# Performance work log

Hardware: AMD Instinct MI355X
Metric: run time of the kernel (lower is better)

Reference implementation:

```python
import jax, jax.numpy as jnp
import numpy as np
import math

DIM = 1024; B = 4; S = 2048; R = 3; K = 256; MAXR = 256; H = 8; HD = DIM // H
THRESH = 0.5; EPS = 1e-5

def _gelu(x):
    return jax.nn.gelu(x, approximate=False)

def _ln(x, g, b):
    m = jnp.mean(x, axis=-1, keepdims=True)
    v = jnp.var(x, axis=-1, keepdims=True)
    return (x - m) * jax.lax.rsqrt(v + EPS) * g + b

def setup_inputs() -> dict:
    key = jax.random.key(0)
    ks = jax.random.split(key, 24)
    sd = 1.0 / math.sqrt(DIM)
    sd2 = 1.0 / math.sqrt(2 * DIM)
    return {
        'x': jax.random.normal(ks[0], (B, S, DIM), jnp.float32),
        'retrieved': jax.random.normal(ks[1], (R, B, K, DIM), jnp.float32),
        # per-retriever query generator MLPs: Linear->GELU->Linear
        'qg_w1': jax.random.normal(ks[2], (R, DIM, DIM), jnp.float32) * sd,
        'qg_b1': jnp.zeros((R, DIM), jnp.float32),
        'qg_w2': jax.random.normal(ks[3], (R, DIM, DIM), jnp.float32) * sd,
        'qg_b2': jnp.zeros((R, DIM), jnp.float32),
        # per-retriever pooler: LayerNorm -> Linear
        'pln_g': jnp.ones((R, DIM), jnp.float32),
        'pln_b': jnp.zeros((R, DIM), jnp.float32),
        'pool_w': jax.random.normal(ks[4], (R, DIM, DIM), jnp.float32) * sd,
        'pool_b': jnp.zeros((R, DIM), jnp.float32),
        # relevance scorer: Linear(2d,d/2)->GELU->Linear(d/2,1)->Sigmoid
        'rel_w1': jax.random.normal(ks[5], (2 * DIM, DIM // 2), jnp.float32) * sd2,
        'rel_b1': jnp.zeros((DIM // 2,), jnp.float32),
        'rel_w2': jax.random.normal(ks[6], (DIM // 2, 1), jnp.float32) * (1.0 / math.sqrt(DIM // 2)),
        'rel_b2': jnp.zeros((1,), jnp.float32),
        # fusion MultiheadAttention: stacked q/k/v in-proj + out-proj
        'in_w': jax.random.normal(ks[7], (3, DIM, DIM), jnp.float32) * sd,
        'in_b': jnp.zeros((3, DIM), jnp.float32),
        'out_w': jax.random.normal(ks[8], (DIM, DIM), jnp.float32) * sd,
        'out_b': jnp.zeros((DIM,), jnp.float32),
        # fusion LayerNorm
        'fln_g': jnp.ones((DIM,), jnp.float32),
        'fln_b': jnp.zeros((DIM,), jnp.float32),
    }

def reference(x, retrieved, qg_w1, qg_b1, qg_w2, qg_b2, pln_g, pln_b, pool_w, pool_b,
              rel_w1, rel_b1, rel_w2, rel_b2, in_w, in_b, out_w, out_b, fln_g, fln_b):
    # ---- query generation: per-retriever MLP + self-attn pooling ----
    qf = _gelu(jnp.einsum('bsd,rde->rbse', x, qg_w1) + qg_b1[:, None, None, :])
    qf = jnp.einsum('rbsd,rde->rbse', qf, qg_w2) + qg_b2[:, None, None, :]  # [R,B,S,D]
    attn = jax.nn.softmax(jnp.einsum('rbsd,rbtd->rbst', qf, qf) / math.sqrt(DIM), axis=-1)
    pooled = jnp.einsum('rbst,rbtd->rbsd', attn, qf).mean(axis=2)  # [R,B,D]
    pooled = _ln(pooled, pln_g[:, None, :], pln_b[:, None, :])
    queries = jnp.einsum('rbd,rde->rbe', pooled, pool_w) + pool_b[:, None, :]  # [R,B,D]
    # ---- relevance scoring of retrieved tokens against queries ----
    q_exp = jnp.broadcast_to(queries[:, :, None, :], (R, B, K, DIM))
    pairs = jnp.concatenate([retrieved, q_exp], axis=-1)  # [R,B,K,2D]
    h = _gelu(pairs @ rel_w1 + rel_b1)
    rel = jax.nn.sigmoid((h @ rel_w2 + rel_b2)[..., 0])  # [R,B,K]
    # ---- threshold mask + per-batch top-k across all retrievers ----
    cand_tok = jnp.transpose(retrieved, (1, 0, 2, 3)).reshape(B, R * K, DIM)
    cand_rel = jnp.transpose(rel, (1, 0, 2)).reshape(B, R * K)
    valid = cand_rel >= THRESH
    masked_rel = jnp.where(valid, cand_rel, -jnp.inf)
    _, top_idx = jax.lax.top_k(masked_rel, MAXR)  # [B,MAXR]
    sel_tok = jnp.take_along_axis(cand_tok, top_idx[..., None], axis=1)  # [B,MAXR,D]
    key_valid = jnp.take_along_axis(valid, top_idx, axis=1)  # [B,MAXR]
    any_valid = jnp.any(key_valid, axis=-1)  # [B]
    # ---- fusion: cross-attention x -> selected tokens, residual + LN ----
    q = (x @ in_w[0] + in_b[0]).reshape(B, S, H, HD)
    k = (sel_tok @ in_w[1] + in_b[1]).reshape(B, MAXR, H, HD)
    v = (sel_tok @ in_w[2] + in_b[2]).reshape(B, MAXR, H, HD)
    scores = jnp.einsum('bshd,bthd->bhst', q, k) / math.sqrt(HD)
    scores = jnp.where(key_valid[:, None, None, :], scores, -1e9)
    a = jax.nn.softmax(scores, axis=-1)
    fused = jnp.einsum('bhst,bthd->bshd', a, v).reshape(B, S, DIM) @ out_w + out_b
    enhanced = _ln(x + fused, fln_g, fln_b)
    return jnp.where(any_valid[:, None, None], enhanced, x)
```

## Files before the change

kernel.cpp:

```cpp
#include <hip/hip_runtime.h>
#include <math.h>


typedef unsigned short u16;
typedef unsigned int   u32;
typedef __attribute__((ext_vector_type(8))) short short8;
typedef __attribute__((ext_vector_type(4))) float f32x4;
typedef __attribute__((ext_vector_type(4))) u16  u16x4;

__device__ __forceinline__ float b2f(u16 u){ union{float f;u32 i;} x; x.i=((u32)u)<<16; return x.f; }
__device__ __forceinline__ u16 f2b(float f){ union{float f;u32 i;} x; x.f=f; u32 r=x.i+0x7fffu+((x.i>>16)&1u); return (u16)(r>>16); }
__device__ __forceinline__ float gelu_f(float v){ return 0.5f*v*(1.f+erff(v*0.70710678118654752f)); }

__device__ __forceinline__ void load_lds16(const u16* g, u16* l){
  __builtin_amdgcn_global_load_lds((const __attribute__((address_space(1))) u32*)g,
                                   (__attribute__((address_space(3))) u32*)l, 16, 0, 0);
}

__device__ __forceinline__ float waveRedSum(float v){
  #pragma unroll
  for (int o=32;o>0;o>>=1) v += __shfl_xor(v,o);
  return v;
}
__device__ __forceinline__ float waveRedMax(float v){
  #pragma unroll
  for (int o=32;o>0;o>>=1) v = fmaxf(v, __shfl_xor(v,o));
  return v;
}
__device__ float blockRedSum(float v){
  __shared__ float tmp[17];
  const int lane = threadIdx.x&63, wv = threadIdx.x>>6, nw = blockDim.x>>6;
  v = waveRedSum(v);
  __syncthreads();
  if (lane==0) tmp[wv]=v;
  __syncthreads();
  if (threadIdx.x==0){ float s=tmp[0]; for(int i=1;i<nw;i++) s+=tmp[i]; tmp[16]=s; }
  __syncthreads();
  return tmp[16];
}
__device__ float blockRedMax(float v){
  __shared__ float tmp[17];
  const int lane = threadIdx.x&63, wv = threadIdx.x>>6, nw = blockDim.x>>6;
  v = waveRedMax(v);
  __syncthreads();
  if (lane==0) tmp[wv]=v;
  __syncthreads();
  if (threadIdx.x==0){ float s=tmp[0]; for(int i=1;i<nw;i++) s=fmaxf(s,tmp[i]); tmp[16]=s; }
  __syncthreads();
  return tmp[16];
}

enum { EPI_NONE=0, EPI_BIAS=1, EPI_SCALE=3, EPI_VT=5 };

template<int EPI>
__global__ __launch_bounds__(512,4)
void gemm_nt(const u16* __restrict__ Ag, long long lda, long long sA1, long long sA2,
             const u16* __restrict__ Bg, long long ldb, long long sB1, long long sB2,
             u16* __restrict__ Cg, long long ldc, long long sC1, long long sC2,
             const float* __restrict__ bias, long long sBias,
             float scale, int K, int H)
{
  __shared__ u16 As[2*4096];
  __shared__ u16 Bs[2*4096];
  const int z  = blockIdx.z;
  const int zb = z / H, zh = z - zb*H;
  const u16* A = Ag + zb*sA1 + zh*sA2;
  const u16* B = Bg + zb*sB1 + zh*sB2;
  const int m0 = blockIdx.y*128, n0 = blockIdx.x*128;
  const int t  = threadIdx.x;
  const int lane = t & 63, wv = t >> 6;
  const int wm = (wv>>1)*32, wn = (wv&1)*64;

  const u16* ga0 = A + (long long)(m0 + (t>>2))*lda + (t&3)*8;
  const u16* gb0 = B + (long long)(n0 + (t>>2))*ldb + (t&3)*8;
  u16* lA0 = As + t*8;
  u16* lB0 = Bs + t*8;

  f32x4 acc[2][4];
  #pragma unroll
  for (int i=0;i<2;i++)
    #pragma unroll
    for (int j=0;j<4;j++) acc[i][j] = (f32x4){0.f,0.f,0.f,0.f};

  const short8* arp = (const short8*)(As + (wm + (lane&15))*32 + ((lane>>4)*8));
  const short8* brp = (const short8*)(Bs + (wn + (lane&15))*32 + ((lane>>4)*8));

  #define STAGE_NT(bo) do{ \
    load_lds16(ga0, lA0+(bo)); \
    load_lds16(gb0, lB0+(bo)); \
    ga0 += 32; gb0 += 32; }while(0)

  const int nk = K >> 5;
  STAGE_NT(0);
  asm volatile("s_waitcnt vmcnt(0)" ::: "memory");
  __builtin_amdgcn_s_barrier();
  int cur = 0;
  for (int kk = 0; kk < nk; ++kk) {
    if (kk+1 < nk) STAGE_NT((cur^1)*4096);
    const int boS = cur*512;
    short8 af[2], bfr[4];
    #pragma unroll
    for (int i=0;i<2;i++) af[i]  = arp[boS + i*64];
    #pragma unroll
    for (int j=0;j<4;j++) bfr[j] = brp[boS + j*64];
    #pragma unroll
    for (int i=0;i<2;i++)
      #pragma unroll
      for (int j=0;j<4;j++)
        acc[i][j] = __builtin_amdgcn_mfma_f32_16x16x32_bf16(af[i], bfr[j], acc[i][j], 0, 0, 0);
    asm volatile("s_waitcnt vmcnt(0)" ::: "memory");
    __builtin_amdgcn_s_barrier();
    cur ^= 1;
  }
  #undef STAGE_NT

  u16* C = Cg + zb*sC1 + zh*sC2;
  const float* bz = bias + zb*sBias;
  const int rb0 = m0 + wm + ((lane>>4)<<2);
  const int cb0 = n0 + wn + (lane&15);
  #pragma unroll
  for (int j=0;j<4;j++){
    const int cn = cb0 + j*16;
    float bv = 0.f;
    if constexpr (EPI==EPI_BIAS || EPI==EPI_VT) bv = bz[cn];
    #pragma unroll
    for (int i=0;i<2;i++){
      #pragma unroll
      for (int p=0;p<4;p++){
        const int row = rb0 + i*16 + p;
        float v = acc[i][j][p];
        if constexpr (EPI==EPI_SCALE) v *= scale;
        if constexpr (EPI==EPI_BIAS)  v += bv;
        if constexpr (EPI==EPI_VT) {
          v += bv;
          const int bb = row>>8, tt = row&255, hh = cn>>7, dd = cn&127;
          C[((long long)((bb*8+hh)*128+dd)<<8) + tt] = f2b(v);
        } else {
          C[(long long)row*ldc + cn] = f2b(v);
        }
      }
    }
  }
}

enum { SP_GELU_SPLIT=0, SP_BIAS_SPLIT=1, SP_SCALE_F32=2, SP_QBG_F32=3, SP_SCALE_STATS=4 };

template<int EPI>
__global__ __launch_bounds__(512,4)
void gemm_nt_split(const u16* __restrict__ Ah_, const u16* __restrict__ Al_, long long lda, long long sAz,
                   const u16* __restrict__ Bh_, const u16* __restrict__ Bl_, long long ldb, long long sBz,
                   void* __restrict__ C0, void* __restrict__ C1, long long ldc, long long sCz,
                   const float* __restrict__ bias, float scale, int K,
                   float* __restrict__ pm, float* __restrict__ ps)
{
  __shared__ u16 AsH[2*4096];
  __shared__ u16 AsL[2*4096];
  __shared__ u16 BsH[2*4096];
  __shared__ u16 BsL[2*4096];
  const int z = blockIdx.z;
  const int m0 = blockIdx.y*128, n0 = blockIdx.x*128;
  const int t  = threadIdx.x;
  const int lane = t & 63, wv = t >> 6;
  const int wm = (wv>>1)*32, wn = (wv&1)*64;

  const long long arow = (long long)z*sAz + (long long)(m0 + (t>>2))*lda + (t&3)*8;
  const long long brow = (long long)z*sBz + (long long)(n0 + (t>>2))*ldb + (t&3)*8;
  const u16* gah0 = Ah_ + arow;
  const u16* gal0 = Al_ + arow;
  const u16* gbh0 = Bh_ + brow;
  const u16* gbl0 = Bl_ + brow;
  u16* lAh0 = AsH + t*8;  u16* lAl0 = AsL + t*8;
  u16* lBh0 = BsH + t*8;  u16* lBl0 = BsL + t*8;

  f32x4 acc[2][4];
  #pragma unroll
  for (int i=0;i<2;i++)
    #pragma unroll
    for (int j=0;j<4;j++) acc[i][j] = (f32x4){0.f,0.f,0.f,0.f};

  const int foff = (lane&15)*32 + ((lane>>4)*8);
  const short8* arh = (const short8*)(AsH + wm*32 + foff);
  const short8* arl = (const short8*)(AsL + wm*32 + foff);
  const short8* brh = (const short8*)(BsH + wn*32 + foff);
  const short8* brl = (const short8*)(BsL + wn*32 + foff);

  #define STAGE_SP(bo) do{ \
    load_lds16(gah0, lAh0+(bo)); load_lds16(gal0, lAl0+(bo)); \
    load_lds16(gbh0, lBh0+(bo)); load_lds16(gbl0, lBl0+(bo)); \
    gah0 += 32; gal0 += 32; gbh0 += 32; gbl0 += 32; }while(0)

  const int nk = K >> 5;
  STAGE_SP(0);
  asm volatile("s_waitcnt vmcnt(0)" ::: "memory");
  __builtin_amdgcn_s_barrier();
  int cur = 0;
  for (int kk = 0; kk < nk; ++kk) {
    if (kk+1 < nk) STAGE_SP((cur^1)*4096);
    const int boS = cur*512;
    short8 fah[2], fal[2], fbh[4], fbl[4];
    #pragma unroll
    for (int i=0;i<2;i++){ fah[i]=arh[boS+i*64]; fal[i]=arl[boS+i*64]; }
    #pragma unroll
    for (int j=0;j<4;j++){ fbh[j]=brh[boS+j*64]; fbl[j]=brl[boS+j*64]; }
    #pragma unroll
    for (int i=0;i<2;i++)
      #pragma unroll
      for (int j=0;j<4;j++){
        acc[i][j] = __builtin_amdgcn_mfma_f32_16x16x32_bf16(fal[i], fbh[j], acc[i][j], 0, 0, 0);
        acc[i][j] = __builtin_amdgcn_mfma_f32_16x16x32_bf16(fah[i], fbl[j], acc[i][j], 0, 0, 0);
        acc[i][j] = __builtin_amdgcn_mfma_f32_16x16x32_bf16(fah[i], fbh[j], acc[i][j], 0, 0, 0);
      }
    asm volatile("s_waitcnt vmcnt(0)" ::: "memory");
    __builtin_amdgcn_s_barrier();
    cur ^= 1;
  }
  #undef STAGE_SP

  const int rb0 = m0 + wm + ((lane>>4)<<2);
  const int cb0 = n0 + wn + (lane&15);
  #pragma unroll
  for (int j=0;j<4;j++){
    const int cn = cb0 + j*16;
    float bv = 0.f;
    if constexpr (EPI==SP_GELU_SPLIT || EPI==SP_BIAS_SPLIT) bv = bias[cn];
    #pragma unroll
    for (int i=0;i<2;i++){
      #pragma unroll
      for (int p=0;p<4;p++){
        const int row = rb0 + i*16 + p;
        float v = acc[i][j][p];
        const long long o = (long long)z*sCz + (long long)row*ldc + cn;
        if constexpr (EPI==SP_GELU_SPLIT || EPI==SP_BIAS_SPLIT){
          v += bv;
          if constexpr (EPI==SP_GELU_SPLIT) v = gelu_f(v);
          const u16 h = f2b(v);
          ((u16*)C0)[o] = h;
          ((u16*)C1)[o] = f2b(v - b2f(h));
        }
        if constexpr (EPI==SP_SCALE_F32 || EPI==SP_SCALE_STATS) ((float*)C0)[o] = v*scale;
        if constexpr (EPI==SP_QBG_F32)   ((float*)C0)[o] = gelu_f(v + bias[(row>>8)*512 + cn]);
      }
    }
  }

  if constexpr (EPI==SP_SCALE_STATS){
    const int g = blockIdx.x*2 + (wv&1);
    #pragma unroll
    for (int i=0;i<2;i++){
      #pragma unroll
      for (int p=0;p<4;p++){
        float mx = -3.4e38f;
        #pragma unroll
        for (int j=0;j<4;j++) mx = fmaxf(mx, acc[i][j][p]*scale);
        #pragma unroll
        for (int o=1;o<16;o<<=1) mx = fmaxf(mx, __shfl_xor(mx,o));
        float sm = 0.f;
        #pragma unroll
        for (int j=0;j<4;j++) sm += expf(acc[i][j][p]*scale - mx);
        #pragma unroll
        for (int o=1;o<16;o<<=1) sm += __shfl_xor(sm,o);
        if ((lane&15)==0){
          const int row = rb0 + i*16 + p;
          const long long pi = ((long long)z*2048 + row)*32 + g;
          pm[pi] = mx; ps[pi] = sm;
        }
      }
    }
  }
}

__global__ __launch_bounds__(256)
void merge_stats(const float* __restrict__ pm, const float* __restrict__ ps,
                 float* __restrict__ m0o, float* __restrict__ d0o,
                 float* __restrict__ m1o, float* __restrict__ d1o){
  const int wv = threadIdx.x>>6, lane = threadIdx.x&63;
  const int row = blockIdx.x*8 + wv*2 + (lane>>5);
  const int g = lane & 31;
  const long long pi = (long long)row*32 + g;
  const float mg = pm[pi];
  float m = mg;
  #pragma unroll
  for (int o=1;o<32;o<<=1) m = fmaxf(m, __shfl_xor(m,o));
  float s = ps[pi] * expf(mg - m);
  #pragma unroll
  for (int o=1;o<32;o<<=1) s += __shfl_xor(s,o);
  if (g==0){
    if (row < 2048){ m0o[row]=m; d0o[row]=s; }
    else           { m1o[row-2048]=m; d1o[row-2048]=s; }
  }
}

__global__ void transpose_w(const float* __restrict__ in, u16* __restrict__ out, int rows, int cols){
  __shared__ float tl[32][33];
  const long long zo = (long long)blockIdx.z*rows*cols;
  const int c0 = blockIdx.x*32, r0 = blockIdx.y*32;
  const int tx = threadIdx.x, ty = threadIdx.y;
  #pragma unroll
  for (int yy=ty; yy<32; yy+=8) tl[yy][tx] = in[zo + (long long)(r0+yy)*cols + (c0+tx)];
  __syncthreads();
  #pragma unroll
  for (int yy=ty; yy<32; yy+=8) out[zo + (long long)(c0+yy)*rows + (r0+tx)] = f2b(tl[tx][yy]);
}

__global__ void split_transpose_w(const float* __restrict__ in, u16* __restrict__ outH,
                                  u16* __restrict__ outL, int rows, int cols){
  __shared__ float tl[32][33];
  const long long zo = (long long)blockIdx.z*rows*cols;
  const int c0 = blockIdx.x*32, r0 = blockIdx.y*32;
  const int tx = threadIdx.x, ty = threadIdx.y;
  #pragma unroll
  for (int yy=ty; yy<32; yy+=8) tl[yy][tx] = in[zo + (long long)(r0+yy)*cols + (c0+tx)];
  __syncthreads();
  #pragma unroll
  for (int yy=ty; yy<32; yy+=8){
    const float v = tl[tx][yy];
    const u16 h = f2b(v);
    const long long o = zo + (long long)(c0+yy)*rows + (r0+tx);
    outH[o] = h;
    outL[o] = f2b(v - b2f(h));
  }
}

__global__ void split_f32_k(const float* __restrict__ in, u16* __restrict__ oh,
                            u16* __restrict__ ol, int n4){
  const int i = blockIdx.x*256 + threadIdx.x;
  if (i < n4){
    const float4 v = ((const float4*)in)[i];
    u16x4 hh, ll;
    hh.x=f2b(v.x); ll.x=f2b(v.x-b2f(hh.x));
    hh.y=f2b(v.y); ll.y=f2b(v.y-b2f(hh.y));
    hh.z=f2b(v.z); ll.z=f2b(v.z-b2f(hh.z));
    hh.w=f2b(v.w); ll.w=f2b(v.w-b2f(hh.w));
    ((u16x4*)oh)[i] = hh;
    ((u16x4*)ol)[i] = ll;
  }
}

__global__ void zero_f32(float* __restrict__ p, int n){
  const int i = blockIdx.x*256 + threadIdx.x;
  if (i < n) p[i] = 0.f;
}

__global__ void init_queries(const float* __restrict__ pb, float* __restrict__ q){
  const int i = blockIdx.x*256 + threadIdx.x;
  if (i < 12288) q[i] = pb[(i>>12)*1024 + (i&1023)];
}
__global__ void init_qpart(const float* __restrict__ rb1, float* __restrict__ qp){
  const int i = blockIdx.x*256 + threadIdx.x;
  if (i < 6144) qp[i] = rb1[i&511];
}

__global__ void ws_report(float* __restrict__ out, int n4, float val){
  const int i = blockIdx.x*256 + threadIdx.x;
  if (i < n4){
    float4 z; z.x = (i==0)? val : 0.f; z.y=0.f; z.z=0.f; z.w=0.f;
    ((float4*)out)[i] = z;
  }
}

__global__ void col_mean2(const float* __restrict__ S, long long sz,
                          const float* __restrict__ m0a, const float* __restrict__ den0,
                          const float* __restrict__ m1a, const float* __restrict__ den1,
                          float* __restrict__ w){
  const int zz = blockIdx.z;
  const float* m   = zz ? m1a : m0a;
  const float* den = zz ? den1 : den0;
  const int tc = blockIdx.x*256 + threadIdx.x;
  const int s0 = blockIdx.y*64;
  const float* p = S + (long long)zz*sz + (long long)s0*2048 + tc;
  float acc = 0.f;
  for (int s=0;s<64;s++)
    acc += expf(p[(long long)s<<11] - m[s0+s]) * (1.0f/den[s0+s]);
  atomicAdd(&w[zz*2048 + tc], acc * (1.f/2048.f));
}

__global__ __launch_bounds__(256)
void pooled_par(const u16* __restrict__ qfh, const u16* __restrict__ qfl,
                const float* __restrict__ w, float* __restrict__ pooled){
  const int b = blockIdx.x, tt0 = blockIdx.y*128;
  const int t = threadIdx.x;
  __shared__ float wsh[128];
  if (t < 128) wsh[t] = w[b*2048 + tt0 + t];
  __syncthreads();
  const long long base = (long long)b*2097152 + (long long)tt0*1024;
  const u16* ph = qfh + base;
  const u16* pl = qfl + base;
  float acc[4] = {0.f,0.f,0.f,0.f};
  for (int s=0; s<128; s++){
    const float wt = wsh[s];
    const long long o = (long long)s*1024;
    #pragma unroll
    for (int k=0;k<4;k++){
      const int dd = t + k*256;
      acc[k] += wt*(b2f(ph[o+dd]) + b2f(pl[o+dd]));
    }
  }
  #pragma unroll
  for (int k=0;k<4;k++) atomicAdd(&pooled[b*1024 + t + k*256], acc[k]);
}

__global__ __launch_bounds__(1024)
void pool_ln(const float* __restrict__ pooled, const float* __restrict__ pg,
             const float* __restrict__ pb, float* __restrict__ plbuf){
  const int z = blockIdx.x, r = z>>2, d = threadIdx.x;
  const float v = pooled[z*1024+d];
  const float mean = blockRedSum(v) * (1.f/1024.f);
  const float df = v - mean;
  const float var = blockRedSum(df*df) * (1.f/1024.f);
  plbuf[z*1024+d] = df*rsqrtf(var+1e-5f)*pg[r*1024+d] + pb[r*1024+d];
}

__global__ __launch_bounds__(256)
void query_accum(const float* __restrict__ plbuf, const float* __restrict__ pw,
                 float* __restrict__ queries){
  const int z = blockIdx.x, r = z>>2, k0 = blockIdx.y*32;
  const int t = threadIdx.x;
  __shared__ float pls[32];
  if (t < 32) pls[t] = plbuf[z*1024 + k0 + t];
  __syncthreads();
  const float* wp = pw + (long long)r*1048576 + (long long)k0*1024;
  float acc[4] = {0.f,0.f,0.f,0.f};
  for (int s=0;s<32;s++){
    const float wv = pls[s];
    #pragma unroll
    for (int c=0;c<4;c++) acc[c] += wv*wp[s*1024 + t + c*256];
  }
  #pragma unroll
  for (int c=0;c<4;c++) atomicAdd(&queries[z*1024 + t + c*256], acc[c]);
}

__global__ __launch_bounds__(256)
void qpart_accum(const float* __restrict__ queries, const float* __restrict__ rw1,
                 float* __restrict__ qpart){
  const int z = blockIdx.x, k0 = blockIdx.y*64;
  const int t = threadIdx.x;
  __shared__ float qs[64];
  if (t < 64) qs[t] = queries[z*1024 + k0 + t];
  __syncthreads();
  const float* wp = rw1 + 1024*512 + (long long)k0*512;
  float acc[2] = {0.f,0.f};
  for (int s=0;s<64;s++){
    const float wv = qs[s];
    #pragma unroll
    for (int c=0;c<2;c++) acc[c] += wv*wp[s*512 + t + c*256];
  }
  #pragma unroll
  for (int c=0;c<2;c++) atomicAdd(&qpart[z*512 + t + c*256], acc[c]);
}

__global__ void rel_score_f32(const float* __restrict__ h, const float* __restrict__ w2,
                              const float* __restrict__ b2p, float* __restrict__ relv){
  const int row = blockIdx.x*4 + (threadIdx.x>>6);
  const int lane = threadIdx.x & 63;
  const float* p = h + (long long)row*512;
  float a = 0.f;
  #pragma unroll
  for (int k=0;k<8;k++){ const int idx = lane + k*64; a += p[idx]*w2[idx]; }
  a = waveRedSum(a);
  if (lane==0){
    const float lg = a + b2p[0];
    relv[row] = 1.f/(1.f+expf(-lg));
  }
}

__global__ __launch_bounds__(768)
void select_topk(const float* __restrict__ relv, int* __restrict__ selidx,
                 int* __restrict__ neff, int* __restrict__ anyv){
  const int b = blockIdx.x, c = threadIdx.x;
  __shared__ float rv[768];
  __shared__ int cnt;
  rv[c] = relv[(((c>>8)*4)+b)*256 + (c&255)];
  if (c==0) cnt = 0;
  __syncthreads();
  const float mine = rv[c];
  const bool valid = (mine >= 0.5f);
  int rank = 0;
  for (int j=0;j<768;j++){
    const float vj = rv[j];
    if (vj >= 0.5f && (vj > mine || (vj == mine && j < c))) rank++;
  }
  if (valid && rank < 256){
    const int s = atomicAdd(&cnt, 1);
    selidx[b*256 + s] = c;
  }
  __syncthreads();
  if (c==0){ neff[b] = cnt; anyv[b] = (cnt>0) ? 1 : 0; }
}

__global__ void gather_sel(const u16* __restrict__ rb16, const int* __restrict__ selidx,
                           const int* __restrict__ neff, u16* __restrict__ seltok){
  const int slot = blockIdx.x, b = blockIdx.y, tid = threadIdx.x;
  uint2 val; val.x=0u; val.y=0u;
  if (slot < neff[b]){
    const int c = selidx[b*256+slot];
    const uint2* src = (const uint2*)(rb16 + (long long)(((c>>8)*4+b)*256 + (c&255))*1024);
    val = src[tid];
  }
  ((uint2*)(seltok + (long long)(b*256+slot)*1024))[tid] = val;
}

__global__ void attn_softmax(u16* __restrict__ S, const int* __restrict__ neff){
  const int ri = blockIdx.x*4 + (threadIdx.x>>6);
  const int lane = threadIdx.x & 63;
  const int b = ri >> 14;
  const int ne = neff[b];
  u16* p = S + (long long)ri*256 + lane*4;
  if (ne == 0){ uint2 zz; zz.x=0u; zz.y=0u; *(uint2*)p = zz; return; }
  uint2 raw = *(const uint2*)p;
  u16 uu[4] = {(u16)(raw.x&0xffffu),(u16)(raw.x>>16),(u16)(raw.y&0xffffu),(u16)(raw.y>>16)};
  float xs[4];
  #pragma unroll
  for (int q2=0;q2<4;q2++){ const int tt = lane*4+q2; xs[q2] = (tt<ne)? b2f(uu[q2]) : -1e30f; }
  float mx = fmaxf(fmaxf(xs[0],xs[1]),fmaxf(xs[2],xs[3]));
  mx = waveRedMax(mx);
  float e[4]; float sm=0.f;
  #pragma unroll
  for (int q2=0;q2<4;q2++){ e[q2] = (lane*4+q2<ne)? expf(xs[q2]-mx) : 0.f; sm += e[q2]; }
  sm = waveRedSum(sm);
  const float inv = 1.f/sm;
  #pragma unroll
  for (int q2=0;q2<4;q2++) uu[q2] = f2b(e[q2]*inv);
  raw.x = (u32)uu[0] | ((u32)uu[1]<<16);
  raw.y = (u32)uu[2] | ((u32)uu[3]<<16);
  *(uint2*)p = raw;
}

__global__ void final_ln(const float* __restrict__ x, const u16* __restrict__ fused,
                         const float* __restrict__ g, const float* __restrict__ bb,
                         const int* __restrict__ anyv, float* __restrict__ out){
  const int row = blockIdx.x; const int b = row>>11; const int tid = threadIdx.x;
  const float4 xv = ((const float4*)(x + (long long)row*1024))[tid];
  const uint2 fv = ((const uint2*)(fused + (long long)row*1024))[tid];
  const float e0 = xv.x + b2f((u16)(fv.x&0xffffu));
  const float e1 = xv.y + b2f((u16)(fv.x>>16));
  const float e2 = xv.z + b2f((u16)(fv.y&0xffffu));
  const float e3 = xv.w + b2f((u16)(fv.y>>16));
  const float mean = blockRedSum(e0+e1+e2+e3) * (1.f/1024.f);
  const float d0=e0-mean, d1=e1-mean, d2=e2-mean, d3=e3-mean;
  const float var = blockRedSum(d0*d0+d1*d1+d2*d2+d3*d3) * (1.f/1024.f);
  const float inv = rsqrtf(var + 1e-5f);
  const float4 gv = ((const float4*)g)[tid];
  const float4 bv = ((const float4*)bb)[tid];
  float4 o;
  if (anyv[b]){
    o.x = d0*inv*gv.x + bv.x; o.y = d1*inv*gv.y + bv.y;
    o.z = d2*inv*gv.z + bv.z; o.w = d3*inv*gv.w + bv.w;
  } else o = xv;
  ((float4*)(out + (long long)row*1024))[tid] = o;
}

extern "C" void kernel_launch(void* const* d_in, const int* in_sizes, int n_in,
                              void* d_out, int out_size, void* d_ws, size_t ws_size,
                              hipStream_t stream) {
  (void)in_sizes; (void)n_in;
  const float* x      = (const float*)d_in[0];
  const float* retr   = (const float*)d_in[1];
  const float* qg_w1  = (const float*)d_in[2];
  const float* qg_b1  = (const float*)d_in[3];
  const float* qg_w2  = (const float*)d_in[4];
  const float* qg_b2  = (const float*)d_in[5];
  const float* pln_g  = (const float*)d_in[6];
  const float* pln_b  = (const float*)d_in[7];
  const float* pool_w = (const float*)d_in[8];
  const float* pool_b = (const float*)d_in[9];
  const float* rel_w1 = (const float*)d_in[10];
  const float* rel_b1 = (const float*)d_in[11];
  const float* rel_w2 = (const float*)d_in[12];
  const float* rel_b2 = (const float*)d_in[13];
  const float* in_w   = (const float*)d_in[14];
  const float* in_b   = (const float*)d_in[15];
  const float* out_w  = (const float*)d_in[16];
  const float* out_b  = (const float*)d_in[17];
  const float* fln_g  = (const float*)d_in[18];
  const float* fln_b  = (const float*)d_in[19];
  float* out = (float*)d_out;
  char* ws = (char*)d_ws;

  const size_t MB = 1u<<20;
  const size_t REQUIRED = 131*MB;
  if (ws_size < REQUIRED){
    ws_report<<<(out_size/4 + 255)/256, 256, 0, stream>>>(out, out_size/4, (float)(ws_size>>20));
    return;
  }

  u16* qg1Th = (u16*)(ws + 0*MB);
  u16* qg1Tl = (u16*)(ws + 6*MB);
  u16* qg2Th = (u16*)(ws + 12*MB);
  u16* qg2Tl = (u16*)(ws + 18*MB);
  u16* xh    = (u16*)(ws + 24*MB);
  u16* xl    = (u16*)(ws + 40*MB);
  u16* qfh   = (u16*)(ws + 56*MB);
  u16* qfl   = (u16*)(ws + 72*MB);
  u16* t1h   = (u16*)(ws + 88*MB);
  u16* t1l   = (u16*)(ws + 104*MB);
  float* scoresA = (float*)(ws + 88*MB);
  float* scoresB = (float*)(ws + 104*MB);
  u16* rh    = (u16*)(ws + 0*MB);
  u16* rl    = (u16*)(ws + 6*MB);
  u16* relTh = (u16*)(ws + 12*MB);
  u16* relTl = (u16*)(ws + 13*MB);
  u16* seltok= (u16*)(ws + 14*MB);
  u16* kbuf  = (u16*)(ws + 16*MB);
  u16* VT    = (u16*)(ws + 18*MB);
  float* hbuf= (float*)(ws + 88*MB);
  u16* inT   = (u16*)(ws + 40*MB);
  u16* outT  = (u16*)(ws + 46*MB);
  u16* qbuf  = (u16*)(ws + 56*MB);
  u16* fused = (u16*)(ws + 72*MB);
  u16* Sattn = (u16*)(ws + 88*MB);
  u16* attnout=(u16*)(ws + 0*MB);
  char* SM = ws + 120*MB;
  float* wbuf    = (float*)(SM);
  float* pooledB = (float*)(SM + 98304);
  float* plbuf   = (float*)(SM + 147456);
  float* queries = (float*)(SM + 196608);
  float* qpart   = (float*)(SM + 245760);
  float* relv    = (float*)(SM + 270336);
  int*   selidx  = (int*)(SM + 282624);
  int*   neff    = (int*)(SM + 286720);
  int*   anyv    = (int*)(SM + 286784);
  float* mrow0   = (float*)(SM + 286848);
  float* drow0   = (float*)(SM + 295040);
  float* mrow1   = (float*)(SM + 303232);
  float* drow1   = (float*)(SM + 311424);
  float* partM   = (float*)(SM + 512*1024);
  float* partS   = (float*)(SM + 1536*1024);

  dim3 b256(256);
  dim3 b512(512);
  dim3 tb(32,8);
  const long long SCZ = (long long)(16*MB)/4;

  split_transpose_w<<<dim3(32,32,3), tb, 0, stream>>>(qg_w1, qg1Th, qg1Tl, 1024, 1024);
  split_transpose_w<<<dim3(32,32,3), tb, 0, stream>>>(qg_w2, qg2Th, qg2Tl, 1024, 1024);
  split_f32_k<<<8192, b256, 0, stream>>>(x, xh, xl, 2097152);
  zero_f32<<<144, b256, 0, stream>>>(wbuf, 36864);

  for (int r = 0; r < 3; r++){
    const long long wo = (long long)r*1048576;
    gemm_nt_split<SP_GELU_SPLIT><<<dim3(8,64,1), b512, 0, stream>>>(
        xh, xl, 1024, 0,  qg1Th+wo, qg1Tl+wo, 1024, 0,
        t1h, t1l, 1024, 0,  qg_b1+r*1024, 1.f, 1024, nullptr, nullptr);
    gemm_nt_split<SP_BIAS_SPLIT><<<dim3(8,64,1), b512, 0, stream>>>(
        t1h, t1l, 1024, 0,  qg2Th+wo, qg2Tl+wo, 1024, 0,
        qfh, qfl, 1024, 0,  qg_b2+r*1024, 1.f, 1024, nullptr, nullptr);
    for (int p2 = 0; p2 < 2; p2++){
      const long long qo = (long long)(p2*2)*2097152;
      gemm_nt_split<SP_SCALE_STATS><<<dim3(16,16,2), b512, 0, stream>>>(
          qfh+qo, qfl+qo, 1024, 2097152,  qfh+qo, qfl+qo, 1024, 2097152,
          scoresA, nullptr, 2048, SCZ,  nullptr, 0.03125f, 1024, partM, partS);
      merge_stats<<<512, b256, 0, stream>>>(partM, partS, mrow0, drow0, mrow1, drow1);
      col_mean2<<<dim3(8,32,2), b256, 0, stream>>>(
          scoresA, SCZ, mrow0, drow0, mrow1, drow1, wbuf + (r*4+p2*2)*2048);
    }
    pooled_par<<<dim3(4,16), b256, 0, stream>>>(qfh, qfl, wbuf + r*8192, pooledB + r*4096);
  }
  pool_ln<<<12, 1024, 0, stream>>>(pooledB, pln_g, pln_b, plbuf);
  init_queries<<<48, b256, 0, stream>>>(pool_b, queries);
  query_accum<<<dim3(12,32), b256, 0, stream>>>(plbuf, pool_w, queries);

  split_f32_k<<<3072, b256, 0, stream>>>(retr, rh, rl, 786432);
  split_transpose_w<<<dim3(16,32,1), tb, 0, stream>>>(rel_w1, relTh, relTl, 1024, 512);
  init_qpart<<<24, b256, 0, stream>>>(rel_b1, qpart);
  qpart_accum<<<dim3(12,16), b256, 0, stream>>>(queries, rel_w1, qpart);
  gemm_nt_split<SP_QBG_F32><<<dim3(4,24,1), b512, 0, stream>>>(
      rh, rl, 1024, 0,  relTh, relTl, 1024, 0,  hbuf, nullptr, 512, 0,  qpart, 1.f, 1024,
      nullptr, nullptr);
  rel_score_f32<<<768, b256, 0, stream>>>(hbuf, rel_w2, rel_b2, relv);

  select_topk<<<4, 768, 0, stream>>>(relv, selidx, neff, anyv);
  gather_sel<<<dim3(256,4), b256, 0, stream>>>(rh, selidx, neff, seltok);

  transpose_w<<<dim3(32,32,3), tb, 0, stream>>>(in_w,  inT,  1024, 1024);
  transpose_w<<<dim3(32,32,1), tb, 0, stream>>>(out_w, outT, 1024, 1024);
  gemm_nt<EPI_BIAS><<<dim3(8,64,1), b512, 0, stream>>>(
      xh,1024,0,0,  inT,1024,0,0,  qbuf,1024,0,0,  in_b,0, 1.f, 1024, 1);
  gemm_nt<EPI_BIAS><<<dim3(8,8,1), b512, 0, stream>>>(
      seltok,1024,0,0,  inT+1048576,1024,0,0,  kbuf,1024,0,0,  in_b+1024,0, 1.f, 1024, 1);
  gemm_nt<EPI_VT><<<dim3(8,8,1), b512, 0, stream>>>(
      seltok,1024,0,0,  inT+2097152,1024,0,0,  VT,0,0,0,  in_b+2048,0, 1.f, 1024, 1);
  gemm_nt<EPI_SCALE><<<dim3(2,16,32), b512, 0, stream>>>(
      qbuf,1024,2097152,128,  kbuf,1024,262144,128,  Sattn,256,4194304,524288,
      (const float*)nullptr,0, 0.08838834764831845f, 128, 8);
  attn_softmax<<<16384, b256, 0, stream>>>(Sattn, neff);
  gemm_nt<EPI_NONE><<<dim3(1,16,32), b512, 0, stream>>>(
      Sattn,256,4194304,524288,  VT,256,262144,32768,  attnout,1024,2097152,128,
      (const float*)nullptr,0, 1.f, 256, 8);
  gemm_nt<EPI_BIAS><<<dim3(8,64,1), b512, 0, stream>>>(
      attnout,1024,0,0,  outT,1024,0,0,  fused,1024,0,0,  out_b,0, 1.f, 1024, 1);
  final_ln<<<8192, b256, 0, stream>>>(x, fused, fln_g, fln_b, anyv, out);
}
```

Measured before the change: 1.297 ms.

## Use 16-wave 1024-thread GEMM blocks with 32x32 per-wave tiles

```diff
diff --git a/kernel.cpp b/kernel.cpp
--- a/kernel.cpp
+++ b/kernel.cpp
@@ -53,7 +53,7 @@
 enum { EPI_NONE=0, EPI_BIAS=1, EPI_SCALE=3, EPI_VT=5 };
 
 template<int EPI>
-__global__ __launch_bounds__(512,4)
+__global__ __launch_bounds__(1024,8)
 void gemm_nt(const u16* __restrict__ Ag, long long lda, long long sA1, long long sA2,
              const u16* __restrict__ Bg, long long ldb, long long sB1, long long sB2,
              u16* __restrict__ Cg, long long ldc, long long sC1, long long sC2,
@@ -69,26 +69,29 @@
   const int m0 = blockIdx.y*128, n0 = blockIdx.x*128;
   const int t  = threadIdx.x;
   const int lane = t & 63, wv = t >> 6;
-  const int wm = (wv>>1)*32, wn = (wv&1)*64;
-
-  const u16* ga0 = A + (long long)(m0 + (t>>2))*lda + (t&3)*8;
-  const u16* gb0 = B + (long long)(n0 + (t>>2))*ldb + (t&3)*8;
-  u16* lA0 = As + t*8;
-  u16* lB0 = Bs + t*8;
-
-  f32x4 acc[2][4];
+  const int wm = (wv>>2)*32, wn = (wv&3)*32;
+
+  const int tt = t & 511;
+  const u16* g0;
+  u16* l0;
+  if (t < 512){
+    g0 = A + (long long)(m0 + (tt>>2))*lda + (tt&3)*8;
+    l0 = As + tt*8;
+  } else {
+    g0 = B + (long long)(n0 + (tt>>2))*ldb + (tt&3)*8;
+    l0 = Bs + tt*8;
+  }
+
+  f32x4 acc[2][2];
   #pragma unroll
   for (int i=0;i<2;i++)
     #pragma unroll
-    for (int j=0;j<4;j++) acc[i][j] = (f32x4){0.f,0.f,0.f,0.f};
+    for (int j=0;j<2;j++) acc[i][j] = (f32x4){0.f,0.f,0.f,0.f};
 
   const short8* arp = (const short8*)(As + (wm + (lane&15))*32 + ((lane>>4)*8));
   const short8* brp = (const short8*)(Bs + (wn + (lane&15))*32 + ((lane>>4)*8));
 
-  #define STAGE_NT(bo) do{ \
-    load_lds16(ga0, lA0+(bo)); \
-    load_lds16(gb0, lB0+(bo)); \
-    ga0 += 32; gb0 += 32; }while(0)
+  #define STAGE_NT(bo) do{ load_lds16(g0, l0+(bo)); g0 += 32; }while(0)
 
   const int nk = K >> 5;
   STAGE_NT(0);
@@ -98,15 +101,15 @@
   for (int kk = 0; kk < nk; ++kk) {
     if (kk+1 < nk) STAGE_NT((cur^1)*4096);
     const int boS = cur*512;
-    short8 af[2], bfr[4];
+    short8 af[2], bfr[2];
     #pragma unroll
     for (int i=0;i<2;i++) af[i]  = arp[boS + i*64];
     #pragma unroll
-    for (int j=0;j<4;j++) bfr[j] = brp[boS + j*64];
+    for (int j=0;j<2;j++) bfr[j] = brp[boS + j*64];
     #pragma unroll
     for (int i=0;i<2;i++)
       #pragma unroll
-      for (int j=0;j<4;j++)
+      for (int j=0;j<2;j++)
         acc[i][j] = __builtin_amdgcn_mfma_f32_16x16x32_bf16(af[i], bfr[j], acc[i][j], 0, 0, 0);
     asm volatile("s_waitcnt vmcnt(0)" ::: "memory");
     __builtin_amdgcn_s_barrier();
@@ -119,7 +122,7 @@
   const int rb0 = m0 + wm + ((lane>>4)<<2);
   const int cb0 = n0 + wn + (lane&15);
   #pragma unroll
-  for (int j=0;j<4;j++){
+  for (int j=0;j<2;j++){
     const int cn = cb0 + j*16;
     float bv = 0.f;
     if constexpr (EPI==EPI_BIAS || EPI==EPI_VT) bv = bz[cn];
@@ -133,8 +136,8 @@
         if constexpr (EPI==EPI_BIAS)  v += bv;
         if constexpr (EPI==EPI_VT) {
           v += bv;
-          const int bb = row>>8, tt = row&255, hh = cn>>7, dd = cn&127;
-          C[((long long)((bb*8+hh)*128+dd)<<8) + tt] = f2b(v);
+          const int bb = row>>8, tt2 = row&255, hh = cn>>7, dd = cn&127;
+          C[((long long)((bb*8+hh)*128+dd)<<8) + tt2] = f2b(v);
         } else {
           C[(long long)row*ldc + cn] = f2b(v);
         }
@@ -146,7 +149,7 @@
 enum { SP_GELU_SPLIT=0, SP_BIAS_SPLIT=1, SP_SCALE_F32=2, SP_QBG_F32=3, SP_SCALE_STATS=4 };
 
 template<int EPI>
-__global__ __launch_bounds__(512,4)
+__global__ __launch_bounds__(1024,8)
 void gemm_nt_split(const u16* __restrict__ Ah_, const u16* __restrict__ Al_, long long lda, long long sAz,
                    const u16* __restrict__ Bh_, const u16* __restrict__ Bl_, long long ldb, long long sBz,
                    void* __restrict__ C0, void* __restrict__ C1, long long ldc, long long sCz,
@@ -161,22 +164,26 @@
   const int m0 = blockIdx.y*128, n0 = blockIdx.x*128;
   const int t  = threadIdx.x;
   const int lane = t & 63, wv = t >> 6;
-  const int wm = (wv>>1)*32, wn = (wv&1)*64;
-
-  const long long arow = (long long)z*sAz + (long long)(m0 + (t>>2))*lda + (t&3)*8;
-  const long long brow = (long long)z*sBz + (long long)(n0 + (t>>2))*ldb + (t&3)*8;
-  const u16* gah0 = Ah_ + arow;
-  const u16* gal0 = Al_ + arow;
-  const u16* gbh0 = Bh_ + brow;
-  const u16* gbl0 = Bl_ + brow;
-  u16* lAh0 = AsH + t*8;  u16* lAl0 = AsL + t*8;
-  u16* lBh0 = BsH + t*8;  u16* lBl0 = BsL + t*8;
-
-  f32x4 acc[2][4];
+  const int wm = (wv>>2)*32, wn = (wv&3)*32;
+
+  const int tt = t & 511;
+  const u16 *g0, *g1;
+  u16 *l0, *l1;
+  if (t < 512){
+    const long long arow = (long long)z*sAz + (long long)(m0 + (tt>>2))*lda + (tt&3)*8;
+    g0 = Ah_ + arow; g1 = Al_ + arow;
+    l0 = AsH + tt*8; l1 = AsL + tt*8;
+  } else {
+    const long long brow = (long long)z*sBz + (long long)(n0 + (tt>>2))*ldb + (tt&3)*8;
+    g0 = Bh_ + brow; g1 = Bl_ + brow;
+    l0 = BsH + tt*8; l1 = BsL + tt*8;
+  }
+
+  f32x4 acc[2][2];
   #pragma unroll
   for (int i=0;i<2;i++)
     #pragma unroll
-    for (int j=0;j<4;j++) acc[i][j] = (f32x4){0.f,0.f,0.f,0.f};
+    for (int j=0;j<2;j++) acc[i][j] = (f32x4){0.f,0.f,0.f,0.f};
 
   const int foff = (lane&15)*32 + ((lane>>4)*8);
   const short8* arh = (const short8*)(AsH + wm*32 + foff);
@@ -185,9 +192,8 @@
   const short8* brl = (const short8*)(BsL + wn*32 + foff);
 
   #define STAGE_SP(bo) do{ \
-    load_lds16(gah0, lAh0+(bo)); load_lds16(gal0, lAl0+(bo)); \
-    load_lds16(gbh0, lBh0+(bo)); load_lds16(gbl0, lBl0+(bo)); \
-    gah0 += 32; gal0 += 32; gbh0 += 32; gbl0 += 32; }while(0)
+    load_lds16(g0, l0+(bo)); load_lds16(g1, l1+(bo)); \
+    g0 += 32; g1 += 32; }while(0)
 
   const int nk = K >> 5;
   STAGE_SP(0);
@@ -197,15 +203,15 @@
   for (int kk = 0; kk < nk; ++kk) {
     if (kk+1 < nk) STAGE_SP((cur^1)*4096);
     const int boS = cur*512;
-    short8 fah[2], fal[2], fbh[4], fbl[4];
+    short8 fah[2], fal[2], fbh[2], fbl[2];
     #pragma unroll
     for (int i=0;i<2;i++){ fah[i]=arh[boS+i*64]; fal[i]=arl[boS+i*64]; }
     #pragma unroll
-    for (int j=0;j<4;j++){ fbh[j]=brh[boS+j*64]; fbl[j]=brl[boS+j*64]; }
+    for (int j=0;j<2;j++){ fbh[j]=brh[boS+j*64]; fbl[j]=brl[boS+j*64]; }
     #pragma unroll
     for (int i=0;i<2;i++)
       #pragma unroll
-      for (int j=0;j<4;j++){
+      for (int j=0;j<2;j++){
         acc[i][j] = __builtin_amdgcn_mfma_f32_16x16x32_bf16(fal[i], fbh[j], acc[i][j], 0, 0, 0);
         acc[i][j] = __builtin_amdgcn_mfma_f32_16x16x32_bf16(fah[i], fbl[j], acc[i][j], 0, 0, 0);
         acc[i][j] = __builtin_amdgcn_mfma_f32_16x16x32_bf16(fah[i], fbh[j], acc[i][j], 0, 0, 0);
@@ -219,7 +225,7 @@
   const int rb0 = m0 + wm + ((lane>>4)<<2);
   const int cb0 = n0 + wn + (lane&15);
   #pragma unroll
-  for (int j=0;j<4;j++){
+  for (int j=0;j<2;j++){
     const int cn = cb0 + j*16;
     float bv = 0.f;
     if constexpr (EPI==SP_GELU_SPLIT || EPI==SP_BIAS_SPLIT) bv = bias[cn];
@@ -244,24 +250,24 @@
   }
 
   if constexpr (EPI==SP_SCALE_STATS){
-    const int g = blockIdx.x*2 + (wv&1);
+    const int g = blockIdx.x*4 + (wv&3);
     #pragma unroll
     for (int i=0;i<2;i++){
       #pragma unroll
       for (int p=0;p<4;p++){
         float mx = -3.4e38f;
         #pragma unroll
-        for (int j=0;j<4;j++) mx = fmaxf(mx, acc[i][j][p]*scale);
+        for (int j=0;j<2;j++) mx = fmaxf(mx, acc[i][j][p]*scale);
         #pragma unroll
         for (int o=1;o<16;o<<=1) mx = fmaxf(mx, __shfl_xor(mx,o));
         float sm = 0.f;
         #pragma unroll
-        for (int j=0;j<4;j++) sm += expf(acc[i][j][p]*scale - mx);
+        for (int j=0;j<2;j++) sm += expf(acc[i][j][p]*scale - mx);
         #pragma unroll
         for (int o=1;o<16;o<<=1) sm += __shfl_xor(sm,o);
         if ((lane&15)==0){
           const int row = rb0 + i*16 + p;
-          const long long pi = ((long long)z*2048 + row)*32 + g;
+          const long long pi = ((long long)z*2048 + row)*64 + g;
           pm[pi] = mx; ps[pi] = sm;
         }
       }
@@ -270,21 +276,17 @@
 }
 
 __global__ __launch_bounds__(256)
-void merge_stats(const float* __restrict__ pm, const float* __restrict__ ps,
-                 float* __restrict__ m0o, float* __restrict__ d0o,
-                 float* __restrict__ m1o, float* __restrict__ d1o){
+void merge_stats64(const float* __restrict__ pm, const float* __restrict__ ps,
+                   float* __restrict__ m0o, float* __restrict__ d0o,
+                   float* __restrict__ m1o, float* __restrict__ d1o){
   const int wv = threadIdx.x>>6, lane = threadIdx.x&63;
-  const int row = blockIdx.x*8 + wv*2 + (lane>>5);
-  const int g = lane & 31;
-  const long long pi = (long long)row*32 + g;
+  const int row = blockIdx.x*4 + wv;
+  const long long pi = (long long)row*64 + lane;
   const float mg = pm[pi];
-  float m = mg;
-  #pragma unroll
-  for (int o=1;o<32;o<<=1) m = fmaxf(m, __shfl_xor(m,o));
+  const float m = waveRedMax(mg);
   float s = ps[pi] * expf(mg - m);
-  #pragma unroll
-  for (int o=1;o<32;o<<=1) s += __shfl_xor(s,o);
-  if (g==0){
+  s = waveRedSum(s);
+  if (lane==0){
     if (row < 2048){ m0o[row]=m; d0o[row]=s; }
     else           { m1o[row-2048]=m; d1o[row-2048]=s; }
   }
@@ -627,7 +629,7 @@
   float* partS   = (float*)(SM + 1536*1024);
 
   dim3 b256(256);
-  dim3 b512(512);
+  dim3 b1024(1024);
   dim3 tb(32,8);
   const long long SCZ = (long long)(16*MB)/4;
 
@@ -638,18 +640,18 @@
 
   for (int r = 0; r < 3; r++){
     const long long wo = (long long)r*1048576;
-    gemm_nt_split<SP_GELU_SPLIT><<<dim3(8,64,1), b512, 0, stream>>>(
+    gemm_nt_split<SP_GELU_SPLIT><<<dim3(8,64,1), b1024, 0, stream>>>(
         xh, xl, 1024, 0,  qg1Th+wo, qg1Tl+wo, 1024, 0,
         t1h, t1l, 1024, 0,  qg_b1+r*1024, 1.f, 1024, nullptr, nullptr);
-    gemm_nt_split<SP_BIAS_SPLIT><<<dim3(8,64,1), b512, 0, stream>>>(
+    gemm_nt_split<SP_BIAS_SPLIT><<<dim3(8,64,1), b1024, 0, stream>>>(
         t1h, t1l, 1024, 0,  qg2Th+wo, qg2Tl+wo, 1024, 0,
         qfh, qfl, 1024, 0,  qg_b2+r*1024, 1.f, 1024, nullptr, nullptr);
     for (int p2 = 0; p2 < 2; p2++){
       const long long qo = (long long)(p2*2)*2097152;
-      gemm_nt_split<SP_SCALE_STATS><<<dim3(16,16,2), b512, 0, stream>>>(
+      gemm_nt_split<SP_SCALE_STATS><<<dim3(16,16,2), b1024, 0, stream>>>(
           qfh+qo, qfl+qo, 1024, 2097152,  qfh+qo, qfl+qo, 1024, 2097152,
           scoresA, nullptr, 2048, SCZ,  nullptr, 0.03125f, 1024, partM, partS);
-      merge_stats<<<512, b256, 0, stream>>>(partM, partS, mrow0, drow0, mrow1, drow1);
+      merge_stats64<<<1024, b256, 0, stream>>>(partM, partS, mrow0, drow0, mrow1, drow1);
       col_mean2<<<dim3(8,32,2), b256, 0, stream>>>(
           scoresA, SCZ, mrow0, drow0, mrow1, drow1, wbuf + (r*4+p2*2)*2048);
     }
@@ -663,7 +665,7 @@
   split_transpose_w<<<dim3(16,32,1), tb, 0, stream>>>(rel_w1, relTh, relTl, 1024, 512);
   init_qpart<<<24, b256, 0, stream>>>(rel_b1, qpart);
   qpart_accum<<<dim3(12,16), b256, 0, stream>>>(queries, rel_w1, qpart);
-  gemm_nt_split<SP_QBG_F32><<<dim3(4,24,1), b512, 0, stream>>>(
+  gemm_nt_split<SP_QBG_F32><<<dim3(4,24,1), b1024, 0, stream>>>(
       rh, rl, 1024, 0,  relTh, relTl, 1024, 0,  hbuf, nullptr, 512, 0,  qpart, 1.f, 1024,
       nullptr, nullptr);
   rel_score_f32<<<768, b256, 0, stream>>>(hbuf, rel_w2, rel_b2, relv);
@@ -673,20 +675,20 @@
 
   transpose_w<<<dim3(32,32,3), tb, 0, stream>>>(in_w,  inT,  1024, 1024);
   transpose_w<<<dim3(32,32,1), tb, 0, stream>>>(out_w, outT, 1024, 1024);
-  gemm_nt<EPI_BIAS><<<dim3(8,64,1), b512, 0, stream>>>(
+  gemm_nt<EPI_BIAS><<<dim3(8,64,1), b1024, 0, stream>>>(
       xh,1024,0,0,  inT,1024,0,0,  qbuf,1024,0,0,  in_b,0, 1.f, 1024, 1);
-  gemm_nt<EPI_BIAS><<<dim3(8,8,1), b512, 0, stream>>>(
+  gemm_nt<EPI_BIAS><<<dim3(8,8,1), b1024, 0, stream>>>(
       seltok,1024,0,0,  inT+1048576,1024,0,0,  kbuf,1024,0,0,  in_b+1024,0, 1.f, 1024, 1);
-  gemm_nt<EPI_VT><<<dim3(8,8,1), b512, 0, stream>>>(
+  gemm_nt<EPI_VT><<<dim3(8,8,1), b1024, 0, stream>>>(
       seltok,1024,0,0,  inT+2097152,1024,0,0,  VT,0,0,0,  in_b+2048,0, 1.f, 1024, 1);
-  gemm_nt<EPI_SCALE><<<dim3(2,16,32), b512, 0, stream>>>(
+  gemm_nt<EPI_SCALE><<<dim3(2,16,32), b1024, 0, stream>>>(
       qbuf,1024,2097152,128,  kbuf,1024,262144,128,  Sattn,256,4194304,524288,
       (const float*)nullptr,0, 0.08838834764831845f, 128, 8);
   attn_softmax<<<16384, b256, 0, stream>>>(Sattn, neff);
-  gemm_nt<EPI_NONE><<<dim3(1,16,32), b512, 0, stream>>>(
+  gemm_nt<EPI_NONE><<<dim3(1,16,32), b1024, 0, stream>>>(
       Sattn,256,4194304,524288,  VT,256,262144,32768,  attnout,1024,2097152,128,
       (const float*)nullptr,0, 1.f, 256, 8);
-  gemm_nt<EPI_BIAS><<<dim3(8,64,1), b512, 0, stream>>>(
+  gemm_nt<EPI_BIAS><<<dim3(8,64,1), b1024, 0, stream>>>(
       attnout,1024,0,0,  outT,1024,0,0,  fused,1024,0,0,  out_b,0, 1.f, 1024, 1);
   final_ln<<<8192, b256, 0, stream>>>(x, fused, fln_g, fln_b, anyv, out);
 }
```

After: 1.307 ms. No clear change (+0.8%).
